# Performance work log

Hardware: AMD Instinct MI355X
Metric: run time of the kernel (lower is better)

## Reference

```python
import jax, jax.numpy as jnp
import numpy as np

COST_W = {'cls': 1.0, 'center': 0.0, 'obj_ness': 0.0, 'giou': 2.0}
IOU_THRES = 0.25
MAX_DYN = 10
EPS = 1e-6
N_PRED, N_GT, N_CLS = 65536, 128, 256


def _to_bbox(centers, sizes):
    # center/size -> (x1,y1,z1,x2,y2,z2)
    return jnp.concatenate([centers - sizes / 2.0, centers + sizes / 2.0], axis=-1)


def _giou_3d(b1, b2):
    # b1 [N,6], b2 [M,6] -> giou [N,M] (axis_aligned_bbox_overlaps_3d, mode='giou')
    vol1 = jnp.prod(b1[:, 3:] - b1[:, :3], axis=-1)  # [N]
    vol2 = jnp.prod(b2[:, 3:] - b2[:, :3], axis=-1)  # [M]
    lt = jnp.maximum(b1[:, None, :3], b2[None, :, :3])  # [N,M,3]
    rb = jnp.minimum(b1[:, None, 3:], b2[None, :, 3:])
    overlap = jnp.prod(jnp.clip(rb - lt, 0.0), axis=-1)  # [N,M]
    union = jnp.maximum(vol1[:, None] + vol2[None, :] - overlap, EPS)
    iou = overlap / union
    elt = jnp.minimum(b1[:, None, :3], b2[None, :, :3])
    erb = jnp.maximum(b1[:, None, 3:], b2[None, :, 3:])
    enclose = jnp.maximum(jnp.prod(jnp.clip(erb - elt, 0.0), axis=-1), EPS)
    return iou - (enclose - union) / enclose


def _lsa(cost):
    # Jonker-Volgenant shortest-augmenting-path LAP (same optimum as
    # scipy.optimize.linear_sum_assignment). cost [n, m], n <= m.
    # Returns col4row[n]: column matched to each row.
    n, m = cost.shape
    u = np.zeros(n, np.float64)
    v = np.zeros(m, np.float64)
    col4row = np.full(n, -1, np.int64)
    row4col = np.full(m, -1, np.int64)
    cost = cost.astype(np.float64)
    for cur in range(n):
        shortest = np.full(m, np.inf)
        path = np.full(m, -1, np.int64)
        SC = np.zeros(m, bool)
        SR = []
        i, min_val, sink = cur, 0.0, -1
        while sink == -1:
            SR.append(i)
            r = min_val + cost[i] - u[i] - v
            upd = (~SC) & (r < shortest)
            shortest = np.where(upd, r, shortest)
            path = np.where(upd, i, path)
            masked = np.where(SC, np.inf, shortest)
            j = int(masked.argmin())
            min_val = masked[j]
            SC[j] = True
            if row4col[j] == -1:
                sink = j
            else:
                i = int(row4col[j])
        u[cur] += min_val
        for i2 in SR:
            if i2 != cur:
                u[i2] += min_val - shortest[col4row[i2]]
        v[SC] -= min_val - shortest[SC]
        j = sink
        while True:
            i2 = int(path[j])
            row4col[j] = i2
            col4row[i2], j = j, col4row[i2]
            if i2 == cur:
                break
    return col4row


def _dynamic_assign(giou, used0, order):
    # Sequential greedy IoU-threshold assignment over gts (ascending max-iou).
    NEG = jnp.float32(-1e9)
    n_pred = giou.shape[0]

    def step(used, gt_idx):
        col = giou[:, gt_idx]
        vals = jnp.where((col > IOU_THRES) & (~used), col, NEG)
        topv, topi = jax.lax.top_k(vals, MAX_DYN)
        valid = topv > NEG
        used = used | jnp.zeros((n_pred,), bool).at[topi].set(valid)
        return used, (jnp.where(valid, topi, -1), jnp.where(valid, gt_idx, -1))

    _, (dp, dg) = jax.lax.scan(step, used0, order)
    return dp.reshape(-1), dg.reshape(-1)  # padded with -1 where invalid


def setup_inputs() -> dict:
    key = jax.random.key(0)
    k = jax.random.split(key, 7)
    return {
        'all_centers': jax.random.normal(k[0], (N_PRED, 3), jnp.float32),
        'all_sizes': jax.random.uniform(k[1], (N_PRED, 3), jnp.float32),
        'all_cls': jax.random.normal(k[2], (N_PRED, N_CLS), jnp.float32),
        'all_objness': jax.random.normal(k[3], (N_PRED,), jnp.float32),
        'gt_centers': jax.random.normal(k[4], (N_GT, 3), jnp.float32),
        'gt_sizes': jax.random.uniform(k[5], (N_GT, 3), jnp.float32),
        'gt_labels': jax.random.randint(k[6], (N_GT,), 0, N_CLS, jnp.int64),
    }


def reference(all_centers, all_sizes, all_cls, all_objness, gt_centers, gt_sizes, gt_labels):
    pred_bbox = _to_bbox(all_centers, all_sizes)
    gt_bbox = _to_bbox(gt_centers, gt_sizes)
    giou = _giou_3d(pred_bbox, gt_bbox)  # [N, M]
    cost_class = -jax.nn.sigmoid(all_cls)[:, gt_labels]  # [N, M]
    cost_center = jnp.sum(jnp.abs(all_centers[:, None, :] - gt_centers[None, :, :]), axis=-1)  # cdist p=1
    cost_obj = -jax.nn.sigmoid(all_objness)[:, None]  # [N, 1]
    total_cost = (COST_W['cls'] * cost_class + COST_W['center'] * cost_center
                  + COST_W['obj_ness'] * cost_obj + COST_W['giou'] * (-giou))
    # Hungarian on transposed cost (M <= N): same optimal pairing as scipy on [N, M].
    col4row = _lsa(np.asarray(jax.device_get(total_cost)).T)
    pred_indices = jnp.asarray(col4row, jnp.int64)       # matched pred per gt
    gt_indices = jnp.arange(gt_labels.shape[0], dtype=jnp.int64)
    used0 = jnp.zeros((giou.shape[0],), bool).at[pred_indices].set(True)
    order = jnp.argsort(jnp.max(giou, axis=0))
    dp, dg = _dynamic_assign(giou, used0, order)
    combined_preds = jnp.concatenate([pred_indices, dp.astype(jnp.int64)])
    combined_gts = jnp.concatenate([gt_indices, dg.astype(jnp.int64)])
    return combined_preds, combined_gts
```

## Files before the change

kernel.cpp:

```cpp
#include <hip/hip_runtime.h>
#include <hip/hip_bf16.h>
#include <math.h>

#define NPRED 65536
#define NGT   128
#define NCLS  256
#define CAP   12288
#define VCAP  160
#define VSLOT 129
#define NLIST 129
#define LSTRIDE 132
#define KEEP  2048
#define KMIN  1418
#define GSPLIT 4
#define GPB   (NGT / GSPLIT)
#define SENT_I 0x7FFFFFFF


__device__ __forceinline__ unsigned f2u(float f) {
    unsigned u = __float_as_uint(f);
    return (u & 0x80000000u) ? ~u : (u | 0x80000000u);
}
__device__ __forceinline__ float u2f(unsigned x) {
    unsigned u = (x & 0x80000000u) ? (x ^ 0x80000000u) : ~x;
    return __uint_as_float(u);
}
__device__ __forceinline__ unsigned long long d2u(double d) {
    unsigned long long u = (unsigned long long)__double_as_longlong(d);
    return (u & 0x8000000000000000ull) ? ~u : (u | 0x8000000000000000ull);
}
__device__ __forceinline__ double u2d(unsigned long long x) {
    unsigned long long u = (x & 0x8000000000000000ull) ? (x ^ 0x8000000000000000ull) : ~x;
    return __longlong_as_double((long long)u);
}

__device__ __forceinline__ float giou3d(
    float pl0, float pl1, float pl2, float ph0, float ph1, float ph2, float pvol,
    float gl0, float gl1, float gl2, float gh0, float gh1, float gh2, float gvol)
{
#pragma clang fp contract(off)
    float c0 = fmaxf(fminf(ph0, gh0) - fmaxf(pl0, gl0), 0.0f);
    float c1 = fmaxf(fminf(ph1, gh1) - fmaxf(pl1, gl1), 0.0f);
    float c2 = fmaxf(fminf(ph2, gh2) - fmaxf(pl2, gl2), 0.0f);
    float overlap = (c0 * c1) * c2;
    float uni = fmaxf((pvol + gvol) - overlap, 1e-6f);
    float iou = overlap / uni;
    float e0 = fmaxf(fmaxf(ph0, gh0) - fminf(pl0, gl0), 0.0f);
    float e1 = fmaxf(fmaxf(ph1, gh1) - fminf(pl1, gl1), 0.0f);
    float e2 = fmaxf(fmaxf(ph2, gh2) - fminf(pl2, gl2), 0.0f);
    float enc = fmaxf((e0 * e1) * e2, 1e-6f);
    return iou - (enc - uni) / enc;
}


__global__ __launch_bounds__(256) void k_gather(
    const float* __restrict__ cls, const int* __restrict__ lab,
    float* __restrict__ costT,
    int* __restrict__ ccnt, unsigned* __restrict__ cmax, int* __restrict__ failFlag)
{
#pragma clang fp contract(off)
    __shared__ float tile[64][NCLS + 1];
    __shared__ int labl[NGT];
    int tid = threadIdx.x;
    int p0 = blockIdx.x * 64;
    if (blockIdx.x == 0) {
        if (tid < NGT) { ccnt[tid] = 0; cmax[tid] = 0u; }
        if (tid == 0) *failFlag = 0;
    }
    if (tid < NGT) labl[tid] = lab[tid];
    for (int it = 0; it < 16; ++it) {
        int row = it * 4 + (tid >> 6);
        int col = (tid & 63) * 4;
        const float4 v = *(const float4*)&cls[(size_t)(p0 + row) * NCLS + col];
        tile[row][col + 0] = v.x; tile[row][col + 1] = v.y;
        tile[row][col + 2] = v.z; tile[row][col + 3] = v.w;
    }
    __syncthreads();
    int lane = tid & 63;
    for (int rep = 0; rep < 32; ++rep) {
        int g = rep * 4 + (tid >> 6);
        float val = tile[lane][labl[g]];
        double s = 1.0 / (1.0 + exp(-(double)val));
        costT[(size_t)g * NPRED + p0 + lane] = -(float)s;
    }
}

__global__ __launch_bounds__(256) void k_cost(
    const float* __restrict__ pc, const float* __restrict__ ps,
    const float* __restrict__ gc, const float* __restrict__ gs,
    float* __restrict__ costT, int* __restrict__ ccnt, unsigned* __restrict__ cmax,
    int2* __restrict__ cpair)
{
#pragma clang fp contract(off)
    __shared__ float gb[GPB][6];
    __shared__ float gvol[GPB];
    __shared__ unsigned smax[GPB];
    __shared__ int cntl[GPB], basel[GPB], curl[GPB];
    int tid = threadIdx.x;
    int lane = tid & 63;
    int g0 = (blockIdx.x & (GSPLIT - 1)) * GPB;
    int p  = (blockIdx.x >> 2) * 256 + tid;

    if (tid < GPB) {
        int g = g0 + tid;
        float c0 = gc[g * 3 + 0], c1 = gc[g * 3 + 1], c2 = gc[g * 3 + 2];
        float s0 = gs[g * 3 + 0], s1 = gs[g * 3 + 1], s2 = gs[g * 3 + 2];
        float l0 = c0 - s0 / 2.0f, l1 = c1 - s1 / 2.0f, l2 = c2 - s2 / 2.0f;
        float h0 = c0 + s0 / 2.0f, h1 = c1 + s1 / 2.0f, h2 = c2 + s2 / 2.0f;
        gb[tid][0] = l0; gb[tid][1] = l1; gb[tid][2] = l2;
        gb[tid][3] = h0; gb[tid][4] = h1; gb[tid][5] = h2;
        gvol[tid] = ((h0 - l0) * (h1 - l1)) * (h2 - l2);
        smax[tid] = 0u; cntl[tid] = 0; curl[tid] = 0;
    }
    __syncthreads();

    float c0 = pc[p * 3 + 0], c1 = pc[p * 3 + 1], c2 = pc[p * 3 + 2];
    float s0 = ps[p * 3 + 0], s1 = ps[p * 3 + 1], s2 = ps[p * 3 + 2];
    float pl0 = c0 - s0 / 2.0f, pl1 = c1 - s1 / 2.0f, pl2 = c2 - s2 / 2.0f;
    float ph0 = c0 + s0 / 2.0f, ph1 = c1 + s1 / 2.0f, ph2 = c2 + s2 / 2.0f;
    float pvol = ((ph0 - pl0) * (ph1 - pl1)) * (ph2 - pl2);

    float gior[GPB];

#pragma unroll
    for (int gg = 0; gg < GPB; ++gg) {
        float gio = giou3d(pl0, pl1, pl2, ph0, ph1, ph2, pvol,
                           gb[gg][0], gb[gg][1], gb[gg][2], gb[gg][3], gb[gg][4], gb[gg][5],
                           gvol[gg]);
        gior[gg] = gio;
        float m = gio;
        for (int off = 32; off; off >>= 1) m = fmaxf(m, __shfl_xor(m, off, 64));
        unsigned long long mask = __ballot(gio > 0.25f);
        if (lane == 0) {
            atomicMax(&smax[gg], f2u(m));
            atomicAdd(&cntl[gg], __popcll(mask));
        }
        size_t ij = (size_t)(g0 + gg) * NPRED + p;
        float ns = costT[ij];
        costT[ij] = ns + (2.0f * (-gio));
    }
    __syncthreads();
    if (tid < GPB) {
        atomicMax(&cmax[g0 + tid], smax[tid]);
        basel[tid] = atomicAdd(&ccnt[g0 + tid], cntl[tid]);
    }
    __syncthreads();

#pragma unroll
    for (int gg = 0; gg < GPB; ++gg) {
        float gio = gior[gg];
        bool cand = (gio > 0.25f);
        unsigned long long mask = __ballot(cand);
        int cnt = __popcll(mask);
        int wo = 0;
        if (lane == 0 && cnt) wo = atomicAdd(&curl[gg], cnt);
        wo = __shfl(wo, 0, 64);
        if (cand) {
            int slot = basel[gg] + wo + __popcll(mask & ((1ull << lane) - 1ull));
            if (slot < CAP)
                cpair[(size_t)(g0 + gg) * CAP + slot] = make_int2(p, __float_as_int(gio));
        }
    }
}

__global__ __launch_bounds__(128) void k_sort(const unsigned* __restrict__ cmax,
                                              int* __restrict__ order) {
    __shared__ unsigned m[NGT];
    int t = threadIdx.x;
    m[t] = cmax[t];
    __syncthreads();
    unsigned mt = m[t];
    int r = 0;
    for (int k = 0; k < NGT; ++k) {
        unsigned mk = m[k];
        if (mk < mt || (mk == mt && k < t)) r++;
    }
    order[r] = t;
}

__global__ __launch_bounds__(256) void k_toprow(
    const float* __restrict__ costT, int2* __restrict__ rowlist)
{
    __shared__ unsigned long long keys[2048];
    __shared__ int hist[256];
    __shared__ unsigned long long sh_prefix;
    __shared__ int sh_rank, sh_cnt, sh_ok;
    int tid = threadIdx.x;
    int row = blockIdx.x;
    const float* crow = costT + (size_t)row * NPRED;

    unsigned long long lv[8];
#pragma unroll
    for (int q = 0; q < 8; ++q) lv[q] = ~0ull;
    const float4* crow4 = (const float4*)crow;
    for (int it = tid; it < NPRED / 4; it += 256) {
        float4 v4 = crow4[it];
        int j = it * 4;
        float vv[4] = {v4.x, v4.y, v4.z, v4.w};
#pragma unroll
        for (int e = 0; e < 4; ++e) {
            unsigned long long key =
                ((unsigned long long)f2u(vv[e]) << 32) | (unsigned)(j + e);
            if (key < lv[7]) {
                unsigned long long c = key;
#pragma unroll
                for (int q = 0; q < 8; ++q) {
                    unsigned long long mx = (c > lv[q]) ? c : lv[q];
                    unsigned long long mn = (c > lv[q]) ? lv[q] : c;
                    lv[q] = mn; c = mx;
                }
            }
        }
    }
#pragma unroll
    for (int q = 0; q < 8; ++q) keys[tid * 8 + q] = lv[q];
    if (tid == 0) sh_ok = 1;
    __syncthreads();

    for (int k = 2; k <= 2048; k <<= 1) {
        for (int j2 = k >> 1; j2 > 0; j2 >>= 1) {
            for (int i = tid; i < 2048; i += 256) {
                int ixj = i ^ j2;
                if (ixj > i) {
                    unsigned long long a = keys[i], b2 = keys[ixj];
                    bool up = ((i & k) == 0);
                    if ((up && a > b2) || (!up && a < b2)) { keys[i] = b2; keys[ixj] = a; }
                }
            }
            __syncthreads();
        }
    }

    unsigned long long thr = keys[NLIST - 1];
    if (lv[7] < thr) sh_ok = 0;
    __syncthreads();

    if (sh_ok) {
        if (tid < NLIST) {
            unsigned long long key = keys[tid];
            rowlist[row * LSTRIDE + tid] =
                make_int2(__float_as_int(u2f((unsigned)(key >> 32))),
                          (int)(unsigned)(key & 0xFFFFFFFFull));
        }
        return;
    }

    if (tid == 0) { sh_prefix = 0ull; sh_rank = NLIST - 1; sh_cnt = 0; }
    __syncthreads();
    for (int d = 7; d >= 0; --d) {
        hist[tid] = 0;
        __syncthreads();
        unsigned long long pref = sh_prefix;
        int sh = (d + 1) * 8;
        for (int j = tid; j < NPRED; j += 256) {
            unsigned long long key = ((unsigned long long)f2u(crow[j]) << 32) | (unsigned)j;
            bool match = (sh >= 64) || ((key >> sh) == (pref >> sh));
            if (match) atomicAdd(&hist[(int)((key >> (d * 8)) & 255ull)], 1);
        }
        __syncthreads();
        if (tid == 0) {
            int rank = sh_rank, cum = 0, b = 0;
            for (; b < 256; ++b) { if (cum + hist[b] > rank) break; cum += hist[b]; }
            sh_prefix = pref | ((unsigned long long)b << (d * 8));
            sh_rank = rank - cum;
        }
        __syncthreads();
    }
    unsigned long long thr2 = sh_prefix;
    for (int j = tid; j < NPRED; j += 256) {
        unsigned long long key = ((unsigned long long)f2u(crow[j]) << 32) | (unsigned)j;
        if (key <= thr2) { int s = atomicAdd(&sh_cnt, 1); keys[s] = key; }
    }
    __syncthreads();
    if (tid >= sh_cnt) keys[tid] = ~0ull;
    __syncthreads();
    for (int k = 2; k <= 256; k <<= 1) {
        for (int j2 = k >> 1; j2 > 0; j2 >>= 1) {
            int i = tid, ixj = i ^ j2;
            if (ixj > i) {
                unsigned long long a = keys[i], b2 = keys[ixj];
                bool up = ((i & k) == 0);
                if ((up && a > b2) || (!up && a < b2)) { keys[i] = b2; keys[ixj] = a; }
            }
            __syncthreads();
        }
    }
    if (tid < NLIST) {
        unsigned long long key = keys[tid];
        rowlist[row * LSTRIDE + tid] =
            make_int2(__float_as_int(u2f((unsigned)(key >> 32))),
                      (int)(unsigned)(key & 0xFFFFFFFFull));
    }
}

__global__ __launch_bounds__(64) void k_lsa_sparse(
    const float* __restrict__ costT, const int2* __restrict__ rowlist,
    int* __restrict__ failFlag,
    unsigned* __restrict__ usedbits, int* __restrict__ out)
{
#pragma clang fp contract(off)
    __shared__ float  costV[NGT][VSLOT];
    __shared__ double u_l[NGT];
    __shared__ int    c4r[NGT];
    __shared__ int    slot4row[NGT];
    __shared__ int    headpos[NGT];
    __shared__ int    colidV[VCAP];
    __shared__ double vV[VCAP], shortV[VCAP];
    __shared__ int    pathV[VCAP], r4cV[VCAP];
    __shared__ unsigned char SCV[VCAP];
    __shared__ int    SRr[VCAP];
    __shared__ double headv[VCAP];
    __shared__ int    headj[VCAP];
    __shared__ unsigned vbits[2048];
    __shared__ int S_bi, S_sink, S_nSR, S_nV, S_fail, S_pendrow, S_pendpos;
    __shared__ double S_mv, S_pendmv;

    int lane = threadIdx.x;
    for (int w = lane; w < 2048; w += 64) vbits[w] = 0u;
    for (int r = lane; r < NGT; r += 64) {
        u_l[r] = 0.0; c4r[r] = -1; slot4row[r] = -1; headpos[r] = 0;
    }
    if (lane == 0) { S_nV = 0; S_fail = 0; }
    __syncthreads();

    for (int cur = 0; cur < NGT; ++cur) {
        int nV0 = S_nV;
        for (int k = lane; k < nV0; k += 64) { shortV[k] = INFINITY; pathV[k] = -1; SCV[k] = 0; }
        if (lane == 0) {
            S_bi = cur; S_sink = -1; S_mv = 0.0;
            SRr[0] = cur; S_nSR = 1;
            S_pendrow = cur; S_pendpos = 0; S_pendmv = 0.0;
        }
        __syncthreads();

        while (true) {
            int prow = S_pendrow;
            int pp   = S_pendpos;
            double pmv = S_pendmv;
            int bi = S_bi; double mv = S_mv; int nV = S_nV; int s = S_nSR;

            int pos = headpos[prow];
            int i0 = pos + lane;
            int2 e0 = (i0 < NLIST) ? rowlist[prow * LSTRIDE + i0]
                                   : make_int2(0, SENT_I);

            double ui = u_l[bi];
            double bv = (double)INFINITY; int bj = SENT_I, bp = SENT_I, baux = -1, bisv = 0;
            for (int k = lane; k < nV; k += 64) {
                if (!SCV[k]) {
                    double c = (double)costV[bi][k];
                    double r = ((mv + c) - ui) - vV[k];
                    if (r < shortV[k]) { shortV[k] = r; pathV[k] = bi; }
                    double sval = shortV[k]; int scol = colidV[k];
                    if (sval < bv || (sval == bv && scol < bj)) {
                        bv = sval; bj = scol; bp = SENT_I; baux = k; bisv = 1;
                    }
                }
            }
            for (int p = lane; p < s; p += 64) {
                if (p == pp) continue;
                double hv = headv[p]; int hj = headj[p];
                if (hv < bv || (hv == bv && (hj < bj || (hj == bj && p < bp)))) {
                    bv = hv; bj = hj; bp = p; baux = p; bisv = 0;
                }
            }

            int hcol = SENT_I; float hval = 0.0f;
            {
                int c0 = e0.y;
                bool fresh = (i0 < NLIST) && !((vbits[c0 >> 5] >> (c0 & 31)) & 1u);
                unsigned long long m0 = __ballot(fresh);
                if (m0) {
                    int fl = __ffsll(m0) - 1;
                    hcol = __shfl(c0, fl, 64);
                    hval = __shfl(__int_as_float(e0.x), fl, 64);
                    pos += fl;
                } else {
                    pos += 64;
                    while (pos < NLIST) {
                        int i = pos + lane;
                        int2 e = (i < NLIST) ? rowlist[prow * LSTRIDE + i] : make_int2(0, SENT_I);
                        int c = e.y;
                        bool fr = (i < NLIST) && !((vbits[c >> 5] >> (c & 31)) & 1u);
                        unsigned long long m = __ballot(fr);
                        if (m) {
                            int fl = __ffsll(m) - 1;
                            hcol = __shfl(c, fl, 64);
                            hval = __shfl(__int_as_float(e.x), fl, 64);
                            pos += fl;
                            break;
                        }
                        pos += 64;
                    }
                }
            }
            double pend_headv = (hcol == SENT_I) ? (double)INFINITY
                                : ((pmv + (double)hval) - u_l[prow]);
            if (pend_headv < bv ||
                (pend_headv == bv && (hcol < bj || (hcol == bj && pp < bp)))) {
                bv = pend_headv; bj = hcol; bp = pp; baux = pp; bisv = 0;
            }

            {
                unsigned long long vkey = d2u(bv);
                unsigned long long mkey = vkey;
#pragma unroll
                for (int off = 1; off < 64; off <<= 1) {
                    unsigned long long o = __shfl_xor(mkey, off, 64);
                    if (o < mkey) mkey = o;
                }
                unsigned long long tiedm = __ballot(vkey == mkey);
                int W;
                if (__popcll(tiedm) > 1) {
                    unsigned long long tkey = (vkey == mkey)
                        ? (((unsigned long long)(unsigned)bj << 32) | (unsigned)bp)
                        : ~0ull;
                    unsigned long long mt = tkey;
#pragma unroll
                    for (int off = 1; off < 64; off <<= 1) {
                        unsigned long long o = __shfl_xor(mt, off, 64);
                        if (o < mt) mt = o;
                    }
                    W = __ffsll(__ballot(tkey == mt)) - 1;
                } else {
                    W = __ffsll(tiedm) - 1;
                }
                bv = u2d(mkey);
                bj = __shfl(bj, W, 64);
                baux = __shfl(baux, W, 64);
                bisv = __shfl(bisv, W, 64);
            }

            if (lane == 0) {
                headpos[prow] = pos;
                headv[pp] = pend_headv; headj[pp] = hcol;
                S_mv = bv;
                if (bisv) {
                    SCV[baux] = 1;
                    int nr = r4cV[baux];
                    SRr[s] = nr;
                    headv[s] = (double)INFINITY; headj[s] = SENT_I;
                    S_pendrow = nr; S_pendpos = s; S_pendmv = bv;
                    S_nSR = s + 1; S_bi = nr;
                } else {
                    int k2 = S_nV;
                    if (k2 >= VCAP) S_fail = 1;
                    else {
                        colidV[k2] = bj; vV[k2] = 0.0; shortV[k2] = bv;
                        pathV[k2] = SRr[baux]; SCV[k2] = 1; r4cV[k2] = -1;
                        vbits[bj >> 5] |= (1u << (bj & 31));
                        S_nV = k2 + 1;
                        S_sink = bj;
                    }
                }
            }
            __syncthreads();
            if (S_sink >= 0 || S_fail) break;
        }
        if (S_fail) break;

        int snew = S_nV - 1;
        int cnew = S_sink;
        float pfa = costT[(size_t)lane * NPRED + cnew];
        float pfb = costT[(size_t)(lane + 64) * NPRED + cnew];

        double mvf = S_mv;
        int nVn = S_nV;
        for (int k = lane; k < nVn; k += 64)
            if (SCV[k]) vV[k] -= (mvf - shortV[k]);
        if (lane == 0) {
            u_l[cur] += mvf;
            int s = S_nSR;
            for (int q = 1; q < s; ++q) {
                int i2 = SRr[q];
                u_l[i2] += mvf - shortV[slot4row[i2]];
            }
            int jslot = S_nV - 1;
            while (true) {
                int i2 = pathV[jslot];
                r4cV[jslot] = i2;
                int oldslot = (c4r[i2] >= 0) ? slot4row[i2] : -1;
                c4r[i2] = colidV[jslot];
                slot4row[i2] = jslot;
                if (i2 == cur) break;
                jslot = oldslot;
            }
        }
        costV[lane][snew]      = pfa;
        costV[lane + 64][snew] = pfb;
        __syncthreads();
    }

    if (lane == 0 && S_fail) *failFlag = 1;
    __syncthreads();
    if (!S_fail) {
        for (int w = lane; w < 2048; w += 64) usedbits[w] = 0u;
        __syncthreads();
        for (int r = lane; r < NGT; r += 64) {
            int p = c4r[r];
            atomicOr(&usedbits[p >> 5], 1u << (p & 31));
            out[r] = p;
            out[1408 + r] = r;
        }
    }
}

__global__ __launch_bounds__(1024) void k_lsa_dense(
    const float* __restrict__ costT, const int* __restrict__ failFlag,
    double* __restrict__ v, double* __restrict__ shortest,
    int* __restrict__ path, int* __restrict__ row4col,
    unsigned char* __restrict__ SC, unsigned* __restrict__ usedbits,
    int* __restrict__ out)
{
#pragma clang fp contract(off)
    if (*failFlag == 0) return;
    __shared__ double u_l[NGT];
    __shared__ int    c4r[NGT];
    __shared__ int    SR[NGT + 1];
    __shared__ int    bi, bsink, nSR;
    __shared__ double bmin;
    __shared__ double wval[16];
    __shared__ int    widx[16];
    int tid = threadIdx.x;

    for (int j = tid; j < NPRED; j += 1024) { v[j] = 0.0; row4col[j] = -1; }
    if (tid < NGT) { u_l[tid] = 0.0; c4r[tid] = -1; }
    __syncthreads();

    for (int cur = 0; cur < NGT; ++cur) {
        for (int j = tid; j < NPRED; j += 1024) {
            shortest[j] = (double)INFINITY; path[j] = -1; SC[j] = 0;
        }
        if (tid == 0) { bi = cur; bsink = -1; bmin = 0.0; SR[0] = cur; nSR = 1; }
        __syncthreads();

        while (true) {
            int irow = bi;
            double mv = bmin;
            double ui = u_l[irow];
            const float* crow = costT + (size_t)irow * NPRED;
            double bestv = (double)INFINITY;
            int    bestj = SENT_I;
            for (int j = tid; j < NPRED; j += 1024) {
                if (!SC[j]) {
                    double s = shortest[j];
                    double r = ((mv + (double)crow[j]) - ui) - v[j];
                    if (r < s) { s = r; shortest[j] = r; path[j] = irow; }
                    if (s < bestv || (s == bestv && j < bestj)) { bestv = s; bestj = j; }
                }
            }
            for (int off = 32; off; off >>= 1) {
                double ov = __shfl_down(bestv, off, 64);
                int    oj = __shfl_down(bestj, off, 64);
                if (ov < bestv || (ov == bestv && oj < bestj)) { bestv = ov; bestj = oj; }
            }
            if ((tid & 63) == 0) { wval[tid >> 6] = bestv; widx[tid >> 6] = bestj; }
            __syncthreads();
            if (tid == 0) {
                double bv = wval[0]; int bj = widx[0];
                for (int w = 1; w < 16; ++w) {
                    double ov = wval[w]; int oj = widx[w];
                    if (ov < bv || (ov == bv && oj < bj)) { bv = ov; bj = oj; }
                }
                bmin = bv;
                SC[bj] = 1;
                int r = row4col[bj];
                if (r < 0) { bsink = bj; }
                else       { SR[nSR++] = r; bi = r; }
            }
            __syncthreads();
            if (bsink >= 0) break;
        }

        double mv = bmin;
        for (int j = tid; j < NPRED; j += 1024)
            if (SC[j]) v[j] -= (mv - shortest[j]);
        if (tid == 0) {
            u_l[cur] += mv;
            for (int k = 1; k < nSR; ++k) {
                int i2 = SR[k];
                u_l[i2] += mv - shortest[c4r[i2]];
            }
            int j = bsink;
            while (true) {
                int i2 = path[j];
                row4col[j] = i2;
                int nj = c4r[i2];
                c4r[i2] = j;
                j = nj;
                if (i2 == cur) break;
            }
        }
        __syncthreads();
    }

    for (int w = tid; w < 2048; w += 1024) usedbits[w] = 0u;
    __syncthreads();
    for (int j = tid; j < NPRED; j += 1024)
        if (row4col[j] >= 0) atomicOr(&usedbits[j >> 5], 1u << (j & 31));
    if (tid < NGT) {
        out[tid]        = c4r[tid];
        out[1408 + tid] = tid;
    }
}

__global__ __launch_bounds__(256) void k_prep(
    const int2* __restrict__ cpair, const int* __restrict__ ccnt,
    unsigned long long* __restrict__ scand, int* __restrict__ kcount,
    int* __restrict__ fullflag)
{
    __shared__ int hist[256];
    __shared__ unsigned long long keys[KEEP];
    __shared__ unsigned sh_pref, sh_thresh;
    __shared__ int sh_done, sh_fail, sh_cnt;
    int tid = threadIdx.x;
    int g = blockIdx.x;
    int nc = ccnt[g]; if (nc > CAP) nc = CAP;
    const int2* src = cpair + (size_t)g * CAP;

    unsigned thresh = 0;
    if (nc > KEEP - 1) {
        if (tid == 0) { sh_pref = 0; sh_done = 0; sh_fail = 0; }
        __syncthreads();
        int above = 0;
        for (int byt = 3; byt >= 0; --byt) {
            hist[tid] = 0;
            __syncthreads();
            unsigned pref = sh_pref;
            for (int c = tid; c < nc; c += 256) {
                unsigned u = f2u(__int_as_float(src[c].y));
                if (byt == 3 || (u >> ((byt + 1) * 8)) == (pref >> ((byt + 1) * 8)))
                    atomicAdd(&hist[(u >> (byt * 8)) & 255], 1);
            }
            __syncthreads();
            if (tid == 0) {
                int cum = 0, B = 0, kept = 0, abnew = above;
                for (int b = 255; b >= 0; --b) {
                    if (above + cum + hist[b] >= KMIN) {
                        B = b; kept = above + cum + hist[b]; abnew = above + cum; break;
                    }
                    cum += hist[b];
                }
                if (kept <= KEEP - 1) { sh_thresh = sh_pref | ((unsigned)B << (byt * 8)); sh_done = 1; }
                else {
                    above = abnew;
                    sh_pref = sh_pref | ((unsigned)B << (byt * 8));
                    if (byt == 0) sh_fail = 1;
                }
            }
            __syncthreads();
            if (sh_done || sh_fail) break;
        }
        if (sh_fail) {
            if (tid == 0) { fullflag[g] = 1; kcount[g] = 0; }
            return;
        }
        thresh = sh_thresh;
    }
    if (tid == 0) sh_cnt = 0;
    __syncthreads();
    for (int c = tid; c < nc; c += 256) {
        unsigned u = f2u(__int_as_float(src[c].y));
        if (u >= thresh) {
            int slot = atomicAdd(&sh_cnt, 1);
            keys[slot] = ((unsigned long long)(~u) << 32) | (unsigned)src[c].x;
        }
    }
    __syncthreads();
    int kept = sh_cnt;
    for (int i = tid; i < KEEP; i += 256) if (i >= kept) keys[i] = ~0ull;
    __syncthreads();
    for (int k = 2; k <= KEEP; k <<= 1) {
        for (int j = k >> 1; j > 0; j >>= 1) {
            for (int i = tid; i < KEEP; i += 256) {
                int ixj = i ^ j;
                if (ixj > i) {
                    unsigned long long a = keys[i], b = keys[ixj];
                    bool up = ((i & k) == 0);
                    if ((up && a > b) || (!up && a < b)) { keys[i] = b; keys[ixj] = a; }
                }
            }
            __syncthreads();
        }
    }
    for (int i = tid; i < KEEP; i += 256) scand[(size_t)g * KEEP + i] = keys[i];
    if (tid == 0) { kcount[g] = kept; fullflag[g] = 0; }
}

__global__ __launch_bounds__(64) void k_dyn2(
    const int* __restrict__ order, const int* __restrict__ kcount,
    const unsigned long long* __restrict__ scand, const int* __restrict__ fullflag,
    const int* __restrict__ ccnt, const int2* __restrict__ cpair,
    const unsigned* __restrict__ usedbits_g, const int* __restrict__ failFlag,
    int* __restrict__ out)
{
    __shared__ unsigned bits[2048];
    int lane = threadIdx.x;
    for (int w = lane; w < 2048; w += 64) bits[w] = usedbits_g[w];
    __syncthreads();
    bool globalFull = (*failFlag != 0);

    for (int k = 0; k < NGT; ++k) {
        int gt = order[k];
        int got = 0;
        if (!globalFull && fullflag[gt] == 0) {
            int kept = kcount[gt];
            int base = 0;
            while (got < 10 && base < kept) {
                int i = base + lane;
                unsigned long long key = (i < kept) ? scand[(size_t)gt * KEEP + i] : ~0ull;
                int p = (int)(unsigned)(key & 0xFFFFFFFFull);
                bool ok = (key != ~0ull) && !((bits[p >> 5] >> (p & 31)) & 1u);
                unsigned long long mask = __ballot(ok);
                int need = 10 - got;
                int pre = __popcll(mask & ((1ull << lane) - 1ull));
                if (ok && pre < need) {
                    out[128 + k * 10 + got + pre] = p;
                    out[1408 + 128 + k * 10 + got + pre] = gt;
                    atomicOr(&bits[p >> 5], 1u << (p & 31));
                }
                int tot = __popcll(mask);
                got += (tot < need) ? tot : need;
                base += 64;
                __syncthreads();
            }
        } else {
            int nc = ccnt[gt]; if (nc > CAP) nc = CAP;
            float lv[10]; int li[10];
#pragma unroll
            for (int q = 0; q < 10; ++q) { lv[q] = -1e30f; li[q] = SENT_I; }
            for (int c = lane; c < nc; c += 64) {
                int2 pr = cpair[(size_t)gt * CAP + c];
                int p = pr.x;
                if ((bits[p >> 5] >> (p & 31)) & 1u) continue;
                float cv = __int_as_float(pr.y); int ci = p;
#pragma unroll
                for (int q = 0; q < 10; ++q) {
                    bool b = (cv > lv[q]) || (cv == lv[q] && ci < li[q]);
                    float tv = b ? lv[q] : cv; int ti = b ? li[q] : ci;
                    if (b) { lv[q] = cv; li[q] = ci; }
                    cv = tv; ci = ti;
                }
            }
#pragma unroll
            for (int q = 0; q < 10; ++q) {
                float mo = lv[0]; int mj = li[0];
#pragma unroll
                for (int off = 1; off < 64; off <<= 1) {
                    float ov = __shfl_xor(mo, off, 64);
                    int oj = __shfl_xor(mj, off, 64);
                    if (ov > mo || (ov == mo && oj < mj)) { mo = ov; mj = oj; }
                }
                bool valid = (mj != SENT_I);
                if (valid && li[0] == mj) {
#pragma unroll
                    for (int t = 0; t < 9; ++t) { lv[t] = lv[t + 1]; li[t] = li[t + 1]; }
                    lv[9] = -1e30f; li[9] = SENT_I;
                }
                if (lane == q) {
                    out[128 + k * 10 + q] = valid ? mj : -1;
                    out[1408 + 128 + k * 10 + q] = valid ? gt : -1;
                    if (valid) atomicOr(&bits[mj >> 5], 1u << (mj & 31));
                }
            }
            got = 10;
            __syncthreads();
        }
        for (int q = got + lane; q < 10; q += 64) {
            out[128 + k * 10 + q] = -1;
            out[1408 + 128 + k * 10 + q] = -1;
        }
        __syncthreads();
    }
}


extern "C" void kernel_launch(void* const* d_in, const int* in_sizes, int n_in,
                              void* d_out, int out_size, void* d_ws, size_t ws_size,
                              hipStream_t stream) {
    const float* pc  = (const float*)d_in[0];
    const float* ps  = (const float*)d_in[1];
    const float* cls = (const float*)d_in[2];
    const float* gc  = (const float*)d_in[4];
    const float* gs  = (const float*)d_in[5];
    const int*   lab = (const int*)d_in[6];

    char* ws = (char*)d_ws;
    float*         costT    = (float*)(ws + 0);
    unsigned long long* scand = (unsigned long long*)(ws + 0);
    int2*          rowlist  = (int2*)(ws + 33554432);
    double*        v        = (double*)(ws + 33554432);
    double*        shortest = (double*)(ws + 34078720);
    int*           path     = (int*)(ws + 34603008);
    int*           row4col  = (int*)(ws + 34865152);
    unsigned char* SC       = (unsigned char*)(ws + 35127296);
    int*           kcount   = (int*)(ws + 35192832);
    int*           fullflag = (int*)(ws + 35193344);
    int*           ccnt     = (int*)(ws + 35193856);
    unsigned*      cmax     = (unsigned*)(ws + 35194368);
    int*           order    = (int*)(ws + 35194880);
    int*           failFlag = (int*)(ws + 35195392);
    unsigned*      usedbits = (unsigned*)(ws + 35195904);
    int2*          cpair    = (int2*)(ws + 35204096);

    int* out = (int*)d_out;

    hipLaunchKernelGGL(k_gather, dim3(NPRED / 64), dim3(256), 0, stream,
                       cls, lab, costT, ccnt, cmax, failFlag);
    hipLaunchKernelGGL(k_cost, dim3((NPRED / 256) * GSPLIT), dim3(256), 0, stream,
                       pc, ps, gc, gs, costT, ccnt, cmax, cpair);
    hipLaunchKernelGGL(k_sort, dim3(1), dim3(128), 0, stream, cmax, order);
    hipLaunchKernelGGL(k_toprow, dim3(NGT), dim3(256), 0, stream, costT, rowlist);
    hipLaunchKernelGGL(k_lsa_sparse, dim3(1), dim3(64), 0, stream,
                       costT, rowlist, failFlag, usedbits, out);
    hipLaunchKernelGGL(k_lsa_dense, dim3(1), dim3(1024), 0, stream,
                       costT, failFlag, v, shortest, path, row4col, SC, usedbits, out);
    hipLaunchKernelGGL(k_prep, dim3(NGT), dim3(256), 0, stream,
                       cpair, ccnt, scand, kcount, fullflag);
    hipLaunchKernelGGL(k_dyn2, dim3(1), dim3(64), 0, stream,
                       order, kcount, scand, fullflag, ccnt, cpair, usedbits, failFlag, out);
}
```

Baseline: 736.1 us.

## Keep sparse LSA column state in registers and fold order sort into toprow

Moves the per-column shortest, v, column id and scanned flags of the single-wave sparse LSA kernel from shared memory into two register slots per lane (VCAP ≤ 128 via lane and lane+64). The serial dual-variable update loop on lane 0 becomes a parallel shuffle-based update across lanes. The separate k_sort launch is merged into k_toprow as an extra block, removing one kernel launch. The aim is to cut shared-memory traffic and serial work on the latency-bound single-wave critical path. The register mapping assumes VCAP (160) never exceeds 128 in practice, which adds correctness risk for slots 128..159.

```diff
diff --git a/kernel.cpp b/kernel.cpp
--- a/kernel.cpp
+++ b/kernel.cpp
@@ -163,30 +163,32 @@
     }
 }
 
-__global__ __launch_bounds__(128) void k_sort(const unsigned* __restrict__ cmax,
-                                              int* __restrict__ order) {
-    __shared__ unsigned m[NGT];
-    int t = threadIdx.x;
-    m[t] = cmax[t];
-    __syncthreads();
-    unsigned mt = m[t];
-    int r = 0;
-    for (int k = 0; k < NGT; ++k) {
-        unsigned mk = m[k];
-        if (mk < mt || (mk == mt && k < t)) r++;
-    }
-    order[r] = t;
-}
-
 __global__ __launch_bounds__(256) void k_toprow(
-    const float* __restrict__ costT, int2* __restrict__ rowlist)
+    const float* __restrict__ costT, int2* __restrict__ rowlist,
+    const unsigned* __restrict__ cmax, int* __restrict__ order)
 {
     __shared__ unsigned long long keys[2048];
     __shared__ int hist[256];
     __shared__ unsigned long long sh_prefix;
     __shared__ int sh_rank, sh_cnt, sh_ok;
+    __shared__ unsigned msort[NGT];
     int tid = threadIdx.x;
     int row = blockIdx.x;
+
+    if (row == NGT) {
+        if (tid < NGT) msort[tid] = cmax[tid];
+        __syncthreads();
+        if (tid < NGT) {
+            unsigned mt = msort[tid];
+            int r = 0;
+            for (int k = 0; k < NGT; ++k) {
+                unsigned mk = msort[k];
+                if (mk < mt || (mk == mt && k < tid)) r++;
+            }
+            order[r] = tid;
+        }
+        return;
+    }
     const float* crow = costT + (size_t)row * NPRED;
 
     unsigned long long lv[8];
@@ -305,9 +307,7 @@
     __shared__ int    slot4row[NGT];
     __shared__ int    headpos[NGT];
     __shared__ int    colidV[VCAP];
-    __shared__ double vV[VCAP], shortV[VCAP];
     __shared__ int    pathV[VCAP], r4cV[VCAP];
-    __shared__ unsigned char SCV[VCAP];
     __shared__ int    SRr[VCAP];
     __shared__ double headv[VCAP];
     __shared__ int    headj[VCAP];
@@ -321,11 +321,17 @@
         u_l[r] = 0.0; c4r[r] = -1; slot4row[r] = -1; headpos[r] = 0;
     }
     if (lane == 0) { S_nV = 0; S_fail = 0; }
+    double short0 = INFINITY, short1 = INFINITY;
+    double v0 = 0.0, v1 = 0.0;
+    int col0 = SENT_I, col1 = SENT_I;
+    int sc0 = 0, sc1 = 0;
     __syncthreads();
 
     for (int cur = 0; cur < NGT; ++cur) {
         int nV0 = S_nV;
-        for (int k = lane; k < nV0; k += 64) { shortV[k] = INFINITY; pathV[k] = -1; SCV[k] = 0; }
+        short0 = INFINITY; short1 = INFINITY; sc0 = 0; sc1 = 0;
+        if (lane < nV0)      pathV[lane]      = -1;
+        if (lane + 64 < nV0) pathV[lane + 64] = -1;
         if (lane == 0) {
             S_bi = cur; S_sink = -1; S_mv = 0.0;
             SRr[0] = cur; S_nSR = 1;
@@ -346,15 +352,23 @@
 
             double ui = u_l[bi];
             double bv = (double)INFINITY; int bj = SENT_I, bp = SENT_I, baux = -1, bisv = 0;
-            for (int k = lane; k < nV; k += 64) {
-                if (!SCV[k]) {
-                    double c = (double)costV[bi][k];
-                    double r = ((mv + c) - ui) - vV[k];
-                    if (r < shortV[k]) { shortV[k] = r; pathV[k] = bi; }
-                    double sval = shortV[k]; int scol = colidV[k];
-                    if (sval < bv || (sval == bv && scol < bj)) {
-                        bv = sval; bj = scol; bp = SENT_I; baux = k; bisv = 1;
-                    }
+            if (lane < nV && !sc0) {
+                double c = (double)costV[bi][lane];
+                double r = ((mv + c) - ui) - v0;
+                if (r < short0) { short0 = r; pathV[lane] = bi; }
+                double sval = short0; int scol = col0;
+                if (sval < bv || (sval == bv && scol < bj)) {
+                    bv = sval; bj = scol; bp = SENT_I; baux = lane; bisv = 1;
+                }
+            }
+            int k1 = lane + 64;
+            if (k1 < nV && !sc1) {
+                double c = (double)costV[bi][k1];
+                double r = ((mv + c) - ui) - v1;
+                if (r < short1) { short1 = r; pathV[k1] = bi; }
+                double sval = short1; int scol = col1;
+                if (sval < bv || (sval == bv && scol < bj)) {
+                    bv = sval; bj = scol; bp = SENT_I; baux = k1; bisv = 1;
                 }
             }
             for (int p = lane; p < s; p += 64) {
@@ -431,25 +445,37 @@
                 bisv = __shfl(bisv, W, 64);
             }
 
-            if (lane == 0) {
-                headpos[prow] = pos;
-                headv[pp] = pend_headv; headj[pp] = hcol;
-                S_mv = bv;
-                if (bisv) {
-                    SCV[baux] = 1;
+            if (bisv) {
+                if ((baux & 63) == lane) {
+                    if (baux & 64) sc1 = 1; else sc0 = 1;
+                }
+                if (lane == 0) {
+                    headpos[prow] = pos;
+                    headv[pp] = pend_headv; headj[pp] = hcol;
+                    S_mv = bv;
                     int nr = r4cV[baux];
                     SRr[s] = nr;
                     headv[s] = (double)INFINITY; headj[s] = SENT_I;
                     S_pendrow = nr; S_pendpos = s; S_pendmv = bv;
                     S_nSR = s + 1; S_bi = nr;
-                } else {
-                    int k2 = S_nV;
-                    if (k2 >= VCAP) S_fail = 1;
+                }
+            } else {
+                if (nV < VCAP) {
+                    if ((nV & 63) == lane) {
+                        if (nV & 64) { col1 = bj; v1 = 0.0; short1 = bv; sc1 = 1; }
+                        else         { col0 = bj; v0 = 0.0; short0 = bv; sc0 = 1; }
+                    }
+                }
+                if (lane == 0) {
+                    headpos[prow] = pos;
+                    headv[pp] = pend_headv; headj[pp] = hcol;
+                    S_mv = bv;
+                    if (nV >= VCAP) S_fail = 1;
                     else {
-                        colidV[k2] = bj; vV[k2] = 0.0; shortV[k2] = bv;
-                        pathV[k2] = SRr[baux]; SCV[k2] = 1; r4cV[k2] = -1;
+                        colidV[nV] = bj;
+                        pathV[nV] = SRr[baux]; r4cV[nV] = -1;
                         vbits[bj >> 5] |= (1u << (bj & 31));
-                        S_nV = k2 + 1;
+                        S_nV = nV + 1;
                         S_sink = bj;
                     }
                 }
@@ -466,16 +492,34 @@
 
         double mvf = S_mv;
         int nVn = S_nV;
-        for (int k = lane; k < nVn; k += 64)
-            if (SCV[k]) vV[k] -= (mvf - shortV[k]);
+        int nSRf = S_nSR;
+        if (lane < nVn && sc0)      v0 -= (mvf - short0);
+        if (lane + 64 < nVn && sc1) v1 -= (mvf - short1);
+
+        {
+            int q = lane;
+            bool act = (q >= 1 && q < nSRf);
+            int i2 = act ? SRr[q] : 0;
+            int sl = act ? slot4row[i2] : 0;
+            double gA = __shfl(short0, sl & 63, 64);
+            double gB = __shfl(short1, sl & 63, 64);
+            double sv = (sl & 64) ? gB : gA;
+            if (act) u_l[i2] += mvf - sv;
+        }
+        {
+            int q = lane + 64;
+            bool act = (q >= 1 && q < nSRf);
+            int i2 = act ? SRr[q] : 0;
+            int sl = act ? slot4row[i2] : 0;
+            double gA = __shfl(short0, sl & 63, 64);
+            double gB = __shfl(short1, sl & 63, 64);
+            double sv = (sl & 64) ? gB : gA;
+            if (act) u_l[i2] += mvf - sv;
+        }
+        if (lane == 0) u_l[cur] += mvf;
+
         if (lane == 0) {
-            u_l[cur] += mvf;
-            int s = S_nSR;
-            for (int q = 1; q < s; ++q) {
-                int i2 = SRr[q];
-                u_l[i2] += mvf - shortV[slot4row[i2]];
-            }
-            int jslot = S_nV - 1;
+            int jslot = snew;
             while (true) {
                 int i2 = pathV[jslot];
                 r4cV[jslot] = i2;
@@ -809,8 +853,8 @@
                        cls, lab, costT, ccnt, cmax, failFlag);
     hipLaunchKernelGGL(k_cost, dim3((NPRED / 256) * GSPLIT), dim3(256), 0, stream,
                        pc, ps, gc, gs, costT, ccnt, cmax, cpair);
-    hipLaunchKernelGGL(k_sort, dim3(1), dim3(128), 0, stream, cmax, order);
-    hipLaunchKernelGGL(k_toprow, dim3(NGT), dim3(256), 0, stream, costT, rowlist);
+    hipLaunchKernelGGL(k_toprow, dim3(NGT + 1), dim3(256), 0, stream,
+                       costT, rowlist, cmax, order);
     hipLaunchKernelGGL(k_lsa_sparse, dim3(1), dim3(64), 0, stream,
                        costT, rowlist, failFlag, usedbits, out);
     hipLaunchKernelGGL(k_lsa_dense, dim3(1), dim3(1024), 0, stream,
```

Result: faster. 711.0 us (-3.4%).
